# Performance work log

Hardware: AMD Instinct MI355X
Metric: run time of the kernel (lower is better)

## Reference

```python
import jax, jax.numpy as jnp
import numpy as np

N_EMBD = 1024
N_HEADS = 16
HEAD_DIM = N_EMBD // N_HEADS


def setup_inputs() -> dict:
    key = jax.random.key(0)
    ks = jax.random.split(key, 6)
    s = 1.0 / np.sqrt(N_EMBD)
    x = jax.random.normal(ks[0], (2, 2048, N_EMBD), dtype=jnp.float32)
    # torch Linear weights are [out, in]; y = x @ W.T
    Wk = jax.random.uniform(ks[1], (N_EMBD, N_EMBD), jnp.float32, -s, s)
    Wq = jax.random.uniform(ks[2], (N_EMBD, N_EMBD), jnp.float32, -s, s)
    Wv = jax.random.uniform(ks[3], (N_EMBD, N_EMBD), jnp.float32, -s, s)
    Wp = jax.random.uniform(ks[4], (N_EMBD, N_EMBD), jnp.float32, -s, s)
    bp = jax.random.uniform(ks[5], (N_EMBD,), jnp.float32, -s, s)
    return {"x": x, "Wq": Wq, "Wk": Wk, "Wv": Wv, "Wp": Wp, "bp": bp}


def reference(x, Wq, Wk, Wv, Wp, bp):
    B, T, C = x.shape
    H, D = N_HEADS, HEAD_DIM
    # projections (torch Linear: x @ W.T), reshape to [B, H, T, D]
    q = (x @ Wq.T).reshape(B, T, H, D).transpose(0, 2, 1, 3)
    k = (x @ Wk.T).reshape(B, T, H, D).transpose(0, 2, 1, 3)
    v = (x @ Wv.T).reshape(B, T, H, D).transpose(0, 2, 1, 3)
    # scaled causal attention, full [B,H,T,T] scores (faithful to original)
    att = jnp.einsum('bhqd,bhkd->bhqk', q, k) * (D ** -0.5)
    causal = jnp.tril(jnp.ones((T, T), dtype=bool))
    att = jnp.where(causal[None, None], att, -jnp.inf)
    att = jax.nn.softmax(att, axis=-1)
    out = jnp.einsum('bhqk,bhkd->bhqd', att, v)
    out = out.transpose(0, 2, 1, 3).reshape(B, T, C)
    return out @ Wp.T + bp
```

## Files before the change

kernel.cpp:

```cpp
#include <hip/hip_runtime.h>

typedef __bf16 bf16;
typedef __bf16 bf16x8 __attribute__((ext_vector_type(8)));
typedef float f32x4 __attribute__((ext_vector_type(4)));

typedef __attribute__((address_space(1))) const void as1_void;
typedef __attribute__((address_space(3))) void as3_void;

#define DEV __device__ __forceinline__
#define NEG_BIG (-1.0e30f)


DEV void async_load16(const void* g, void* l) {
  __builtin_amdgcn_global_load_lds((as1_void*)g, (as3_void*)l, 16, 0, 0);
}
DEV bf16x8 load8(const bf16* p) { bf16x8 v; __builtin_memcpy(&v, p, 16); return v; }
DEV void store8(bf16* p, bf16x8 v) { __builtin_memcpy(p, &v, 16); }

DEV int sniff_bf16(const unsigned short* __restrict__ xr) {
  const int lane = threadIdx.x & 63;
  const unsigned short w = xr[lane * 2];
  const int e = (w >> 7) & 0xFF;
  const bool sane = ((w & 0x7FFF) == 0) || (e >= 97 && e <= 157);
  return __popcll(__ballot(sane)) >= 48;
}

struct ConvArgs {
  const void* src[6];
  bf16* dst[6];
  int n[6];
};

__global__ __launch_bounds__(256) void convert_kernel(ConvArgs a) {
  const int isbf = sniff_bf16((const unsigned short*)a.src[0]);
  const int t = blockIdx.y;
  const int n = a.n[t];
  bf16* d = a.dst[t];
  const int stride = gridDim.x * 256 * 8;
  if (isbf) {
    const bf16* s = (const bf16*)a.src[t];
    for (int i = (blockIdx.x * 256 + threadIdx.x) * 8; i < n; i += stride)
      store8(d + i, load8(s + i));
  } else {
    const float* s = (const float*)a.src[t];
    for (int i = (blockIdx.x * 256 + threadIdx.x) * 8; i < n; i += stride) {
      float tmp[8];
      __builtin_memcpy(tmp, s + i, 32);
      bf16x8 v;
#pragma unroll
      for (int j = 0; j < 8; ++j) v[j] = (bf16)tmp[j];
      store8(d + i, v);
    }
  }
}

DEV void gemm_core_128(const bf16* A, const bf16* W, int K, int m0, int n0,
                       f32x4 (&acc)[4][4]) {
  __shared__ alignas(16) bf16 As[128 * 64];
  __shared__ alignas(16) bf16 Bs[128 * 64];
  const int tid = threadIdx.x;
  const int lane = tid & 63;
  const int wid = tid >> 6;
  const int wm = (wid >> 1) << 6;
  const int wn = (wid & 1) << 6;
  const int lr = lane & 15;
  const int lg = lane >> 4;

  const f32x4 zero = {0.f, 0.f, 0.f, 0.f};
#pragma unroll
  for (int i = 0; i < 4; ++i)
#pragma unroll
    for (int j = 0; j < 4; ++j) acc[i][j] = zero;

  for (int k0 = 0; k0 < K; k0 += 64) {
#pragma unroll
    for (int it = 0; it < 4; ++it) {
      const int lin = it * 256 + tid;
      const int row = lin >> 3;
      const int c8 = (lin & 7) << 3;
      async_load16(A + (size_t)(m0 + row) * K + (size_t)(k0 + c8), As + lin * 8);
      async_load16(W + (size_t)(n0 + row) * K + (size_t)(k0 + c8), Bs + lin * 8);
    }
    __syncthreads();
#pragma unroll
    for (int kk = 0; kk < 64; kk += 32) {
      bf16x8 af[4], bfr[4];
#pragma unroll
      for (int i = 0; i < 4; ++i)
        af[i] = load8(As + (wm + i * 16 + lr) * 64 + kk + lg * 8);
#pragma unroll
      for (int j = 0; j < 4; ++j)
        bfr[j] = load8(Bs + (wn + j * 16 + lr) * 64 + kk + lg * 8);
#pragma unroll
      for (int i = 0; i < 4; ++i)
#pragma unroll
        for (int j = 0; j < 4; ++j)
          acc[i][j] = __builtin_amdgcn_mfma_f32_16x16x32_bf16(af[i], bfr[j], acc[i][j], 0, 0, 0);
    }
    __syncthreads();
  }
}

DEV size_t frag_idx(int row, int col) {
  return ((size_t)(((col >> 5) * 4 + ((row >> 4) & 3)) * 64 + ((col >> 3) & 3) * 16 + (row & 15)) << 3)
         | (size_t)(col & 7);
}

__global__ __launch_bounds__(256) void qkv_proj_kernel(
    const bf16* __restrict__ x, const bf16* __restrict__ Wq,
    const bf16* __restrict__ Wk, const bf16* __restrict__ Wv,
    bf16* __restrict__ q_ws, bf16* __restrict__ k_ws, bf16* __restrict__ vt_ws) {
  const int L = blockIdx.x;
  const int xcd = L & 7;
  const int i2 = L >> 3;
  const int m0 = (xcd * 4 + (i2 & 3)) << 7;
  const int rest = i2 >> 2;
  const int n0 = (rest & 7) << 7;
  const int mode = rest >> 3;
  const bf16* W = (mode == 0) ? Wq : (mode == 1) ? Wk : Wv;
  f32x4 acc[4][4];
  gemm_core_128(x, W, 1024, m0, n0, acc);

  const int tid = threadIdx.x;
  const int lane = tid & 63, wid = tid >> 6;
  const int wm = (wid >> 1) << 6, wn = (wid & 1) << 6;
  const int lr = lane & 15, lg = lane >> 4;
  bf16* out = (mode == 0) ? q_ws : (mode == 1) ? k_ws : vt_ws;
#pragma unroll
  for (int i = 0; i < 4; ++i) {
#pragma unroll
    for (int r = 0; r < 4; ++r) {
      const int m = m0 + wm + i * 16 + lg * 4 + r;
      const int b = m >> 11, t = m & 2047;
#pragma unroll
      for (int j = 0; j < 4; ++j) {
        const int n = n0 + wn + j * 16 + lr;
        const int h = n >> 6, d = n & 63;
        const float v = acc[i][j][r];
        const size_t base = ((size_t)(b * 16 + h) << 17) + ((size_t)(t >> 6) << 12);
        const size_t idx = base + ((mode < 2) ? frag_idx(t & 63, d) : frag_idx(d, t & 63));
        out[idx] = (bf16)v;
      }
    }
  }
}

__global__ __launch_bounds__(256, 2) void attn_kernel(
    const bf16* __restrict__ q_ws, const bf16* __restrict__ k_ws,
    const bf16* __restrict__ vt_ws, bf16* __restrict__ a_ws) {
  const int L = blockIdx.x;
  const int xcd = L & 7;
  const int bh = xcd * 4 + ((L >> 3) & 3);
  const int pr = L >> 5;
  const int tid = threadIdx.x;
  const int lane = tid & 63, w = tid >> 6;
  const int lr = lane & 15, lg = lane >> 4;
  const int fo = lg * 16 + lr;

  __shared__ alignas(16) bf16 Ps[4][16 * 72];
  bf16* ps = &Ps[w][0];

  const size_t hb = (size_t)bh << 17;
  const int b = bh >> 4, h = bh & 15;
  const f32x4 zero = {0.f, 0.f, 0.f, 0.f};

  for (int ph = 0; ph < 2; ++ph) {
    const int qt = ph ? (31 - pr) : pr;
    const size_t qtb = hb + ((size_t)qt << 12);

    bf16x8 aq[2];
#pragma unroll
    for (int c2 = 0; c2 < 2; ++c2)
      aq[c2] = load8(q_ws + qtb + (size_t)(((c2 * 4 + w) * 64 + fo) << 3));

    f32x4 o_acc[4];
#pragma unroll
    for (int j = 0; j < 4; ++j) o_acc[j] = zero;
    float lsum[4] = {0.f, 0.f, 0.f, 0.f};

    auto load_k = [&](bf16x8 (&bk)[4][2], int kt) {
      const size_t ktb = hb + ((size_t)kt << 12);
#pragma unroll
      for (int j = 0; j < 4; ++j)
#pragma unroll
        for (int c2 = 0; c2 < 2; ++c2)
          bk[j][c2] = load8(k_ws + ktb + (size_t)(((c2 * 4 + j) * 64 + fo) << 3));
    };

    auto step = [&](const bf16x8 (&bk)[4][2], int kt, bool diag) {
      const size_t ktb = hb + ((size_t)kt << 12);
      bf16x8 bv[4][2];
#pragma unroll
      for (int j = 0; j < 4; ++j)
#pragma unroll
        for (int c2 = 0; c2 < 2; ++c2)
          bv[j][c2] = load8(vt_ws + ktb + (size_t)(((c2 * 4 + j) * 64 + fo) << 3));

      f32x4 s[4];
#pragma unroll
      for (int j = 0; j < 4; ++j) {
        s[j] = __builtin_amdgcn_mfma_f32_16x16x32_bf16(aq[0], bk[j][0], zero, 0, 0, 0);
        s[j] = __builtin_amdgcn_mfma_f32_16x16x32_bf16(aq[1], bk[j][1], s[j], 0, 0, 0);
      }
      float p[4][4];
#pragma unroll
      for (int j = 0; j < 4; ++j) {
#pragma unroll
        for (int r = 0; r < 4; ++r) {
          float v = s[j][r] * 0.125f;
          if (diag && (j * 16 + lr) > (w * 16 + lg * 4 + r)) v = NEG_BIG;
          p[j][r] = __expf(v);
        }
      }
#pragma unroll
      for (int r = 0; r < 4; ++r)
        lsum[r] += (p[0][r] + p[1][r]) + (p[2][r] + p[3][r]);
#pragma unroll
      for (int j = 0; j < 4; ++j)
#pragma unroll
        for (int r = 0; r < 4; ++r)
          ps[(lg * 4 + r) * 72 + j * 16 + lr] = (bf16)p[j][r];
#pragma unroll
      for (int c2 = 0; c2 < 2; ++c2) {
        const bf16x8 ap = load8(ps + lr * 72 + c2 * 32 + lg * 8);
#pragma unroll
        for (int j = 0; j < 4; ++j)
          o_acc[j] = __builtin_amdgcn_mfma_f32_16x16x32_bf16(ap, bv[j][c2], o_acc[j], 0, 0, 0);
      }
    };

    bf16x8 bkA[4][2], bkB[4][2];
    const int n = qt;
    load_k(bkA, qt);
    if (n > 0) load_k(bkB, 0);
    step(bkA, qt, true);
    int kt = 0;
    while (kt + 1 < n) {
      load_k(bkA, kt + 1);
      step(bkB, kt, false);
      if (kt + 2 < n) load_k(bkB, kt + 2);
      step(bkA, kt + 1, false);
      kt += 2;
    }
    if (kt < n) step(bkB, kt, false);

    float l_i[4];
#pragma unroll
    for (int r = 0; r < 4; ++r) {
      float v = lsum[r];
#pragma unroll
      for (int off = 1; off < 16; off <<= 1) v += __shfl_xor(v, off, 64);
      l_i[r] = v;
    }

#pragma unroll
    for (int r = 0; r < 4; ++r) {
      const int t = qt * 64 + w * 16 + lg * 4 + r;
      const float inv = 1.f / l_i[r];
#pragma unroll
      for (int j = 0; j < 4; ++j) {
        const size_t idx = (((size_t)(b * 2048 + t)) << 10) | (size_t)(h * 64 + j * 16 + lr);
        a_ws[idx] = (bf16)(o_acc[j][r] * inv);
      }
    }
  }
}

__global__ __launch_bounds__(256) void out_proj_kernel(
    const bf16* __restrict__ A, const bf16* __restrict__ Wp,
    const bf16* __restrict__ bp, void* __restrict__ out,
    const unsigned short* __restrict__ xraw) {
  const int L = blockIdx.x;
  const int xcd = L & 7;
  const int i2 = L >> 3;
  const int m0 = (xcd * 4 + (i2 & 3)) << 7;
  const int n0 = (i2 >> 2) << 7;
  f32x4 acc[4][4];
  gemm_core_128(A, Wp, 1024, m0, n0, acc);

  const int tid = threadIdx.x;
  const int lane = tid & 63, wid = tid >> 6;
  const int wm = (wid >> 1) << 6, wn = (wid & 1) << 6;
  const int lr = lane & 15, lg = lane >> 4;
  const int isbf = sniff_bf16(xraw);
#pragma unroll
  for (int i = 0; i < 4; ++i) {
#pragma unroll
    for (int r = 0; r < 4; ++r) {
      const int m = m0 + wm + i * 16 + lg * 4 + r;
#pragma unroll
      for (int j = 0; j < 4; ++j) {
        const int n = n0 + wn + j * 16 + lr;
        const float v = acc[i][j][r] + (float)bp[n];
        const size_t idx = ((size_t)m << 10) | (size_t)n;
        if (isbf) ((bf16*)out)[idx] = (bf16)v;
        else      ((float*)out)[idx] = v;
      }
    }
  }
}

extern "C" void kernel_launch(void* const* d_in, const int* in_sizes, int n_in,
                              void* d_out, int out_size, void* d_ws, size_t ws_size,
                              hipStream_t stream) {
  (void)in_sizes; (void)n_in; (void)out_size;
  if (ws_size < (50u << 20)) return;

  char* ws = (char*)d_ws;
  bf16* q_ws  = (bf16*)(ws);
  bf16* k_ws  = (bf16*)(ws + (8u << 20));
  bf16* vt_ws = (bf16*)(ws + (16u << 20));
  bf16* a_ws  = (bf16*)(ws + (24u << 20));
  bf16* xc    = (bf16*)(ws + (32u << 20));
  bf16* Wqc   = (bf16*)(ws + (40u << 20));
  bf16* Wkc   = (bf16*)(ws + (42u << 20));
  bf16* Wvc   = (bf16*)(ws + (44u << 20));
  bf16* Wpc   = (bf16*)(ws + (46u << 20));
  bf16* bpc   = (bf16*)(ws + (48u << 20));

  ConvArgs ca;
  ca.src[0] = d_in[0]; ca.dst[0] = xc;  ca.n[0] = 4096 * 1024;
  ca.src[1] = d_in[1]; ca.dst[1] = Wqc; ca.n[1] = 1024 * 1024;
  ca.src[2] = d_in[2]; ca.dst[2] = Wkc; ca.n[2] = 1024 * 1024;
  ca.src[3] = d_in[3]; ca.dst[3] = Wvc; ca.n[3] = 1024 * 1024;
  ca.src[4] = d_in[4]; ca.dst[4] = Wpc; ca.n[4] = 1024 * 1024;
  ca.src[5] = d_in[5]; ca.dst[5] = bpc; ca.n[5] = 1024;
  convert_kernel<<<dim3(512, 6), 256, 0, stream>>>(ca);

  qkv_proj_kernel<<<768, 256, 0, stream>>>(xc, Wqc, Wkc, Wvc, q_ws, k_ws, vt_ws);
  attn_kernel<<<512, 256, 0, stream>>>(q_ws, k_ws, vt_ws, a_ws);
  out_proj_kernel<<<256, 256, 0, stream>>>(a_ws, Wpc, bpc, d_out,
                                           (const unsigned short*)d_in[0]);
}
```

Measured before the change: 202.3 us.

## Pre-swizzle GEMM operands into MFMA fragment layout and load directly to registers

The convert kernel now writes x and the weight matrices (and the attention kernel writes its output) in a fragment-tiled layout. Each lane's 16-byte MFMA operand is then contiguous in global memory, so the projection GEMMs load fragments straight into registers and skip the LDS staging and __syncthreads barriers. The QKV block-to-tile mapping is changed for XCD locality, and occupancy hints of 3 are added. In exchange there is no LDS reuse across waves, so each wave fetches its own A/B fragments from global/L2, and the K loop has no explicit prefetch.

```diff
diff --git a/kernel.cpp b/kernel.cpp
--- a/kernel.cpp
+++ b/kernel.cpp
@@ -4,16 +4,10 @@
 typedef __bf16 bf16x8 __attribute__((ext_vector_type(8)));
 typedef float f32x4 __attribute__((ext_vector_type(4)));
 
-typedef __attribute__((address_space(1))) const void as1_void;
-typedef __attribute__((address_space(3))) void as3_void;
-
 #define DEV __device__ __forceinline__
 #define NEG_BIG (-1.0e30f)
 
 
-DEV void async_load16(const void* g, void* l) {
-  __builtin_amdgcn_global_load_lds((as1_void*)g, (as3_void*)l, 16, 0, 0);
-}
 DEV bf16x8 load8(const bf16* p) { bf16x8 v; __builtin_memcpy(&v, p, 16); return v; }
 DEV void store8(bf16* p, bf16x8 v) { __builtin_memcpy(p, &v, 16); }
 
@@ -25,6 +19,12 @@
   return __popcll(__ballot(sane)) >= 48;
 }
 
+DEV size_t frag_off(int row, int k) {
+  const int rt = row >> 7, ks = k >> 6;
+  const int chunk = (((row >> 4) & 7) * 2 + ((k >> 5) & 1)) * 64 + ((k >> 3) & 3) * 16 + (row & 15);
+  return ((((size_t)rt * 16 + (size_t)ks) * 1024 + (size_t)chunk) << 3) | (size_t)(k & 7);
+}
+
 struct ConvArgs {
   const void* src[6];
   bf16* dst[6];
@@ -37,34 +37,29 @@
   const int n = a.n[t];
   bf16* d = a.dst[t];
   const int stride = gridDim.x * 256 * 8;
-  if (isbf) {
-    const bf16* s = (const bf16*)a.src[t];
-    for (int i = (blockIdx.x * 256 + threadIdx.x) * 8; i < n; i += stride)
-      store8(d + i, load8(s + i));
-  } else {
-    const float* s = (const float*)a.src[t];
-    for (int i = (blockIdx.x * 256 + threadIdx.x) * 8; i < n; i += stride) {
+  const bool frag = (t < 5);
+  for (int i = (blockIdx.x * 256 + threadIdx.x) * 8; i < n; i += stride) {
+    bf16x8 v;
+    if (isbf) {
+      v = load8((const bf16*)a.src[t] + i);
+    } else {
       float tmp[8];
-      __builtin_memcpy(tmp, s + i, 32);
-      bf16x8 v;
+      __builtin_memcpy(tmp, (const float*)a.src[t] + i, 32);
 #pragma unroll
       for (int j = 0; j < 8; ++j) v[j] = (bf16)tmp[j];
-      store8(d + i, v);
-    }
-  }
-}
-
-DEV void gemm_core_128(const bf16* A, const bf16* W, int K, int m0, int n0,
-                       f32x4 (&acc)[4][4]) {
-  __shared__ alignas(16) bf16 As[128 * 64];
-  __shared__ alignas(16) bf16 Bs[128 * 64];
-  const int tid = threadIdx.x;
-  const int lane = tid & 63;
-  const int wid = tid >> 6;
-  const int wm = (wid >> 1) << 6;
-  const int wn = (wid & 1) << 6;
-  const int lr = lane & 15;
-  const int lg = lane >> 4;
+    }
+    if (frag) store8(d + frag_off(i >> 10, i & 1023), v);
+    else      store8(d + i, v);
+  }
+}
+
+DEV void gemm_reg_128(const bf16* __restrict__ A, const bf16* __restrict__ W,
+                      int mblk, int nblk, f32x4 (&acc)[4][4]) {
+  const int lane = threadIdx.x & 63, wid = threadIdx.x >> 6;
+  const int wm = (wid >> 1) << 6, wn = (wid & 1) << 6;
+  const int lr = lane & 15, lg = lane >> 4;
+  const int arow = mblk * 128 + wm + lr;
+  const int brow = nblk * 128 + wn + lr;
 
   const f32x4 zero = {0.f, 0.f, 0.f, 0.f};
 #pragma unroll
@@ -72,32 +67,23 @@
 #pragma unroll
     for (int j = 0; j < 4; ++j) acc[i][j] = zero;
 
-  for (int k0 = 0; k0 < K; k0 += 64) {
-#pragma unroll
-    for (int it = 0; it < 4; ++it) {
-      const int lin = it * 256 + tid;
-      const int row = lin >> 3;
-      const int c8 = (lin & 7) << 3;
-      async_load16(A + (size_t)(m0 + row) * K + (size_t)(k0 + c8), As + lin * 8);
-      async_load16(W + (size_t)(n0 + row) * K + (size_t)(k0 + c8), Bs + lin * 8);
-    }
-    __syncthreads();
-#pragma unroll
-    for (int kk = 0; kk < 64; kk += 32) {
-      bf16x8 af[4], bfr[4];
+  for (int ks = 0; ks < 16; ++ks) {
+    bf16x8 af[2][4], bf[2][4];
+#pragma unroll
+    for (int kh = 0; kh < 2; ++kh) {
+      const int k = ks * 64 + kh * 32 + lg * 8;
+#pragma unroll
+      for (int i = 0; i < 4; ++i) af[kh][i] = load8(A + frag_off(arow + i * 16, k));
+#pragma unroll
+      for (int j = 0; j < 4; ++j) bf[kh][j] = load8(W + frag_off(brow + j * 16, k));
+    }
+#pragma unroll
+    for (int kh = 0; kh < 2; ++kh)
 #pragma unroll
       for (int i = 0; i < 4; ++i)
-        af[i] = load8(As + (wm + i * 16 + lr) * 64 + kk + lg * 8);
-#pragma unroll
-      for (int j = 0; j < 4; ++j)
-        bfr[j] = load8(Bs + (wn + j * 16 + lr) * 64 + kk + lg * 8);
-#pragma unroll
-      for (int i = 0; i < 4; ++i)
 #pragma unroll
         for (int j = 0; j < 4; ++j)
-          acc[i][j] = __builtin_amdgcn_mfma_f32_16x16x32_bf16(af[i], bfr[j], acc[i][j], 0, 0, 0);
-    }
-    __syncthreads();
+          acc[i][j] = __builtin_amdgcn_mfma_f32_16x16x32_bf16(af[kh][i], bf[kh][j], acc[i][j], 0, 0, 0);
   }
 }
 
@@ -106,25 +92,25 @@
          | (size_t)(col & 7);
 }
 
-__global__ __launch_bounds__(256) void qkv_proj_kernel(
+__global__ __launch_bounds__(256, 3) void qkv_proj_kernel(
     const bf16* __restrict__ x, const bf16* __restrict__ Wq,
     const bf16* __restrict__ Wk, const bf16* __restrict__ Wv,
     bf16* __restrict__ q_ws, bf16* __restrict__ k_ws, bf16* __restrict__ vt_ws) {
   const int L = blockIdx.x;
   const int xcd = L & 7;
-  const int i2 = L >> 3;
-  const int m0 = (xcd * 4 + (i2 & 3)) << 7;
-  const int rest = i2 >> 2;
-  const int n0 = (rest & 7) << 7;
-  const int mode = rest >> 3;
+  const int idx = L >> 3;
+  const int mblk = (xcd & 3) * 8 + (idx & 7);
+  const int nm = (xcd >> 2) * 12 + (idx >> 3);
+  const int nblk = nm & 7;
+  const int mode = nm >> 3;
   const bf16* W = (mode == 0) ? Wq : (mode == 1) ? Wk : Wv;
   f32x4 acc[4][4];
-  gemm_core_128(x, W, 1024, m0, n0, acc);
-
-  const int tid = threadIdx.x;
-  const int lane = tid & 63, wid = tid >> 6;
+  gemm_reg_128(x, W, mblk, nblk, acc);
+
+  const int lane = threadIdx.x & 63, wid = threadIdx.x >> 6;
   const int wm = (wid >> 1) << 6, wn = (wid & 1) << 6;
   const int lr = lane & 15, lg = lane >> 4;
+  const int m0 = mblk << 7, n0 = nblk << 7;
   bf16* out = (mode == 0) ? q_ws : (mode == 1) ? k_ws : vt_ws;
 #pragma unroll
   for (int i = 0; i < 4; ++i) {
@@ -138,8 +124,8 @@
         const int h = n >> 6, d = n & 63;
         const float v = acc[i][j][r];
         const size_t base = ((size_t)(b * 16 + h) << 17) + ((size_t)(t >> 6) << 12);
-        const size_t idx = base + ((mode < 2) ? frag_idx(t & 63, d) : frag_idx(d, t & 63));
-        out[idx] = (bf16)v;
+        const size_t idx2 = base + ((mode < 2) ? frag_idx(t & 63, d) : frag_idx(d, t & 63));
+        out[idx2] = (bf16)v;
       }
     }
   }
@@ -255,33 +241,33 @@
 
 #pragma unroll
     for (int r = 0; r < 4; ++r) {
-      const int t = qt * 64 + w * 16 + lg * 4 + r;
+      const int mrow = b * 2048 + qt * 64 + w * 16 + lg * 4 + r;
       const float inv = 1.f / l_i[r];
 #pragma unroll
       for (int j = 0; j < 4; ++j) {
-        const size_t idx = (((size_t)(b * 2048 + t)) << 10) | (size_t)(h * 64 + j * 16 + lr);
-        a_ws[idx] = (bf16)(o_acc[j][r] * inv);
-      }
-    }
-  }
-}
-
-__global__ __launch_bounds__(256) void out_proj_kernel(
+        const int col = h * 64 + j * 16 + lr;
+        a_ws[frag_off(mrow, col)] = (bf16)(o_acc[j][r] * inv);
+      }
+    }
+  }
+}
+
+__global__ __launch_bounds__(256, 3) void out_proj_kernel(
     const bf16* __restrict__ A, const bf16* __restrict__ Wp,
     const bf16* __restrict__ bp, void* __restrict__ out,
     const unsigned short* __restrict__ xraw) {
   const int L = blockIdx.x;
   const int xcd = L & 7;
   const int i2 = L >> 3;
-  const int m0 = (xcd * 4 + (i2 & 3)) << 7;
-  const int n0 = (i2 >> 2) << 7;
+  const int mblk = xcd * 4 + (i2 & 3);
+  const int nblk = i2 >> 2;
   f32x4 acc[4][4];
-  gemm_core_128(A, Wp, 1024, m0, n0, acc);
-
-  const int tid = threadIdx.x;
-  const int lane = tid & 63, wid = tid >> 6;
+  gemm_reg_128(A, Wp, mblk, nblk, acc);
+
+  const int lane = threadIdx.x & 63, wid = threadIdx.x >> 6;
   const int wm = (wid >> 1) << 6, wn = (wid & 1) << 6;
   const int lr = lane & 15, lg = lane >> 4;
+  const int m0 = mblk << 7, n0 = nblk << 7;
   const int isbf = sniff_bf16(xraw);
 #pragma unroll
   for (int i = 0; i < 4; ++i) {
```

After: 196.6 us. -2.8%, faster.
